# Kernel optimization log

Measured on AMD Instinct MI355X. Metric: run time of the kernel, lower is better.

Reference implementation:

```python
import jax, jax.numpy as jnp
import numpy as np

NX = 8        # state dim
NU = 8        # control dim (== NX, required by original Fx assignment)
N = 64        # horizon
BATCH = 2048
M = N * NU    # condensed QP size = 512
MAX_ITER = 100
STEP = 0.01
U_MIN, U_MAX = -1.0, 1.0


def _build_buffers():
    rng = np.random.default_rng(0)
    A = rng.standard_normal((NX, NX))
    A /= 1.05 * np.max(np.abs(np.linalg.eigvals(A)))  # stable dynamics
    Bm = 0.1 * rng.standard_normal((NX, NU))
    Q = np.eye(NX)
    R = 0.1 * np.eye(NU)
    Qf = np.eye(NX)
    # Phi[k] = A^k
    Phi = np.zeros((N + 1, NX, NX))
    Phi[0] = np.eye(NX)
    for i in range(N):
        Phi[i + 1] = A @ Phi[i]
    # Gamma[i][:, j*NU:(j+1)*NU] = A^{i-1-j} B  (x_i = A^i x0 + Gamma_i u)
    Gamma = np.zeros((N + 1, NX, M))
    for i in range(1, N + 1):
        for j in range(i):
            Gamma[i, :, j * NU:(j + 1) * NU] = Phi[i - 1 - j] @ Bm
    # Condensed Hessian H_bar = sum_i Gamma_i^T Q Gamma_i + blockdiag(R) + reg
    H = np.zeros((M, M))
    for i in range(1, N):
        H += Gamma[i].T @ Q @ Gamma[i]
    H += Gamma[N].T @ Qf @ Gamma[N]
    H += np.kron(np.eye(N), R)
    H += 1e-6 * np.eye(M)
    return (jnp.asarray(H, jnp.float32), jnp.asarray(Phi, jnp.float32),
            jnp.asarray(Q, jnp.float32))


def setup_inputs() -> dict:
    key = jax.random.key(0)
    k1, k2 = jax.random.split(key)
    x0 = jax.random.normal(k1, (BATCH, NX), dtype=jnp.float32)
    xref = jax.random.normal(k2, (BATCH, N + 1, NX), dtype=jnp.float32)
    H, Phi, Q = _build_buffers()
    return {"x0": x0, "xref": xref, "H": H, "Phi": Phi, "Q": Q}


def reference(x0, xref, H, Phi, Q):
    # Linear term f: Fx_k = -2 * Phi[k] @ Q @ (xref_k - xref_0)   [B, N, NX]
    dx = xref[:, :N] - xref[:, :1]                       # [B, N, NX]
    Fx = -2.0 * jnp.einsum('kij,jl,bkl->bki', Phi[:N], Q, dx)
    f = Fx.reshape(xref.shape[0], M)                     # [B, M]

    # Projected gradient descent QP solve: 100 iterations of
    #   u <- clip(u - step*(H u + f), u_min, u_max)
    def step(u, _):
        grad = u @ H.T + f                               # [B, M]
        u_new = jnp.clip(u - STEP * grad, U_MIN, U_MAX)
        return u_new, None

    u0 = jnp.zeros_like(f)
    u, _ = jax.lax.scan(step, u0, None, length=MAX_ITER)
    return u  # full optimal control sequence [B, N*NU]
```

## Files before the change

kernel.cpp:

```cpp
#include <hip/hip_runtime.h>


typedef unsigned short u16t;
typedef __attribute__((ext_vector_type(8))) short short8;
typedef __attribute__((ext_vector_type(4))) float floatx4;

#define HLDS_BYTES (128 * 520 * 2)
#define UBF_BYTES  (16 * 520 * 2)
#define DYN_LDS    (HLDS_BYTES + UBF_BYTES)

__device__ __forceinline__ u16t f32_to_bf16(float x) {
    unsigned int u = __builtin_bit_cast(unsigned int, x);
    u = (u + 0x7FFFu + ((u >> 16) & 1u)) >> 16;
    return (u16t)u;
}

__global__ void convert_H_bf16(const float* __restrict__ H, u16t* __restrict__ Hb) {
    int idx = blockIdx.x * 256 + threadIdx.x;
    Hb[idx] = f32_to_bf16(H[idx]);
}

#define MFMA(a, b, c) __builtin_amdgcn_mfma_f32_16x16x32_bf16((a), (b), (c), 0, 0, 0)

__global__ __launch_bounds__(512, 2)
void pgd_hybrid_kernel(const float* __restrict__ xref,
                       const float* __restrict__ H,
                       const u16t*  __restrict__ Hb,
                       const float* __restrict__ Phi,
                       const float* __restrict__ Q,
                       float* __restrict__ out)
{
    extern __shared__ __align__(16) char smem[];
    u16t* Hlds = (u16t*)smem;
    u16t (*u_bf)[520] = (u16t(*)[520])(smem + HLDS_BYTES);

    const int tid  = threadIdx.x;
    const int lane = tid & 63;
    const int w    = tid >> 6;
    const int quad = lane >> 4;
    const int lcol = lane & 15;
    const int b0   = blockIdx.x * 16;
    const int colbase = w * 64;

    for (int e = tid; e < 8192; e += 512) {
        int r = e >> 6, c = e & 63;
        *(short8*)&Hlds[r * 520 + c * 8] =
            *(const short8*)&Hb[(long)((r >> 4) * 64 + 32 + (r & 15)) * 512 + c * 8];
    }
    {
        u16t* ub = &u_bf[0][0];
        for (int e = tid; e < 8320; e += 512) ub[e] = 0;
    }

    short8 hfrag[2][16];
    #pragma unroll
    for (int t = 0; t < 2; ++t) {
        const float* hrow = H + (long)(colbase + t * 16 + lcol) * 512;
        #pragma unroll
        for (int ks = 0; ks < 16; ++ks) {
            const float* hp = hrow + ks * 32 + quad * 8;
            short8 fr;
            #pragma unroll
            for (int j = 0; j < 8; ++j) fr[j] = (short)f32_to_bf16(hp[j]);
            hfrag[t][ks] = fr;
        }
    }

    float f_reg[4][4], u_reg[4][4];
    #pragma unroll
    for (int T = 0; T < 4; ++T) {
        int c = colbase + T * 16 + lcol;
        int k = c >> 3, i = c & 7;
        #pragma unroll
        for (int r = 0; r < 4; ++r) {
            int m = quad * 4 + r;
            const float* xr = xref + (long)(b0 + m) * 520;
            float s = 0.f;
            #pragma unroll
            for (int j = 0; j < 8; ++j) {
                float z = 0.f;
                #pragma unroll
                for (int l = 0; l < 8; ++l) z += Q[j * 8 + l] * (xr[k * 8 + l] - xr[l]);
                s += Phi[k * 64 + i * 8 + j] * z;
            }
            f_reg[T][r] = -2.0f * s;
            u_reg[T][r] = 0.0f;
        }
    }
    __syncthreads();

    const u16t* hb3 = Hb + (long)(colbase + 48 + lcol) * 512;
    const u16t* h2  = Hlds + (w * 16 + lcol) * 520;

    short8 s0 = *(const short8*)&hb3[quad * 8];
    short8 s1 = *(const short8*)&hb3[32 + quad * 8];

    for (int it = 0; it < 100; ++it) {
        floatx4 acc[4];
        #pragma unroll
        for (int T = 0; T < 4; ++T) acc[T] = (floatx4){0.f, 0.f, 0.f, 0.f};

        #pragma unroll
        for (int ks = 0; ks < 16; ++ks) {
            short8 a  = *(const short8*)&u_bf[lcol][ks * 32 + quad * 8];
            short8 b2 = *(const short8*)&h2[ks * 32 + quad * 8];
            short8 b3 = s0;
            s0 = s1;
            s1 = *(const short8*)&hb3[(((ks + 2) & 15) * 32 + quad * 8)];
            acc[0] = MFMA(a, hfrag[0][ks], acc[0]);
            acc[1] = MFMA(a, hfrag[1][ks], acc[1]);
            acc[2] = MFMA(a, b2, acc[2]);
            acc[3] = MFMA(a, b3, acc[3]);
        }

        u16t nv[4][4];
        #pragma unroll
        for (int T = 0; T < 4; ++T)
            #pragma unroll
            for (int r = 0; r < 4; ++r) {
                float g  = acc[T][r] + f_reg[T][r];
                float un = u_reg[T][r] - 0.01f * g;
                un = fminf(1.0f, fmaxf(-1.0f, un));
                u_reg[T][r] = un;
                nv[T][r] = f32_to_bf16(un);
            }

        __syncthreads();
        #pragma unroll
        for (int T = 0; T < 4; ++T) {
            int c = colbase + T * 16 + lcol;
            #pragma unroll
            for (int r = 0; r < 4; ++r)
                u_bf[quad * 4 + r][c] = nv[T][r];
        }
        __syncthreads();
    }

    #pragma unroll
    for (int T = 0; T < 4; ++T) {
        int c = colbase + T * 16 + lcol;
        #pragma unroll
        for (int r = 0; r < 4; ++r)
            out[(long)(b0 + quad * 4 + r) * 512 + c] = u_reg[T][r];
    }
}

extern "C" void kernel_launch(void* const* d_in, const int* in_sizes, int n_in,
                              void* d_out, int out_size, void* d_ws, size_t ws_size,
                              hipStream_t stream) {
    const float* xref = (const float*)d_in[1];
    const float* H    = (const float*)d_in[2];
    const float* Phi  = (const float*)d_in[3];
    const float* Q    = (const float*)d_in[4];
    u16t* Hb = (u16t*)d_ws;

    static int attr_done = 0;
    (void)hipFuncSetAttribute((const void*)pgd_hybrid_kernel,
                              hipFuncAttributeMaxDynamicSharedMemorySize, DYN_LDS);
    (void)attr_done;

    convert_H_bf16<<<1024, 256, 0, stream>>>(H, Hb);
    pgd_hybrid_kernel<<<128, 512, DYN_LDS, stream>>>(xref, H, Hb, Phi, Q, (float*)d_out);
}
```

Baseline: 268.5 us.

## Transpose MFMA operands for vectorized u writes, deepen H prefetch ring

After: 331.8 us. 23.6% more time.

```diff
diff --git a/kernel.cpp b/kernel.cpp
--- a/kernel.cpp
+++ b/kernel.cpp
@@ -3,6 +3,7 @@
 
 typedef unsigned short u16t;
 typedef __attribute__((ext_vector_type(8))) short short8;
+typedef __attribute__((ext_vector_type(4))) short short4v;
 typedef __attribute__((ext_vector_type(4))) float floatx4;
 
 #define HLDS_BYTES (128 * 520 * 2)
@@ -23,12 +24,11 @@
 #define MFMA(a, b, c) __builtin_amdgcn_mfma_f32_16x16x32_bf16((a), (b), (c), 0, 0, 0)
 
 __global__ __launch_bounds__(512, 2)
-void pgd_hybrid_kernel(const float* __restrict__ xref,
-                       const float* __restrict__ H,
-                       const u16t*  __restrict__ Hb,
-                       const float* __restrict__ Phi,
-                       const float* __restrict__ Q,
-                       float* __restrict__ out)
+void pgd_kernel9(const float* __restrict__ xref,
+                 const u16t*  __restrict__ Hb,
+                 const float* __restrict__ Phi,
+                 const float* __restrict__ Q,
+                 float* __restrict__ out)
 {
     extern __shared__ __align__(16) char smem[];
     u16t* Hlds = (u16t*)smem;
@@ -52,48 +52,45 @@
         for (int e = tid; e < 8320; e += 512) ub[e] = 0;
     }
 
-    short8 hfrag[2][16];
+    short8 hfragA[2][16];
     #pragma unroll
     for (int t = 0; t < 2; ++t) {
-        const float* hrow = H + (long)(colbase + t * 16 + lcol) * 512;
+        const u16t* hrow = Hb + (long)(colbase + t * 16 + lcol) * 512;
         #pragma unroll
-        for (int ks = 0; ks < 16; ++ks) {
-            const float* hp = hrow + ks * 32 + quad * 8;
-            short8 fr;
-            #pragma unroll
-            for (int j = 0; j < 8; ++j) fr[j] = (short)f32_to_bf16(hp[j]);
-            hfrag[t][ks] = fr;
-        }
+        for (int ks = 0; ks < 16; ++ks)
+            hfragA[t][ks] = *(const short8*)&hrow[ks * 32 + quad * 8];
     }
 
     float f_reg[4][4], u_reg[4][4];
-    #pragma unroll
-    for (int T = 0; T < 4; ++T) {
-        int c = colbase + T * 16 + lcol;
-        int k = c >> 3, i = c & 7;
+    {
+        const float* xr = xref + (long)(b0 + lcol) * 520;
         #pragma unroll
-        for (int r = 0; r < 4; ++r) {
-            int m = quad * 4 + r;
-            const float* xr = xref + (long)(b0 + m) * 520;
-            float s = 0.f;
+        for (int T = 0; T < 4; ++T) {
             #pragma unroll
-            for (int j = 0; j < 8; ++j) {
-                float z = 0.f;
+            for (int r = 0; r < 4; ++r) {
+                int c = colbase + T * 16 + quad * 4 + r;
+                int k = c >> 3, i = c & 7;
+                float s = 0.f;
                 #pragma unroll
-                for (int l = 0; l < 8; ++l) z += Q[j * 8 + l] * (xr[k * 8 + l] - xr[l]);
-                s += Phi[k * 64 + i * 8 + j] * z;
+                for (int j = 0; j < 8; ++j) {
+                    float z = 0.f;
+                    #pragma unroll
+                    for (int l = 0; l < 8; ++l) z += Q[j * 8 + l] * (xr[k * 8 + l] - xr[l]);
+                    s += Phi[k * 64 + i * 8 + j] * z;
+                }
+                f_reg[T][r] = -2.0f * s;
+                u_reg[T][r] = 0.0f;
             }
-            f_reg[T][r] = -2.0f * s;
-            u_reg[T][r] = 0.0f;
         }
     }
     __syncthreads();
 
+    const u16t* h2 = Hlds + (w * 16 + lcol) * 520;
     const u16t* hb3 = Hb + (long)(colbase + 48 + lcol) * 512;
-    const u16t* h2  = Hlds + (w * 16 + lcol) * 520;
-
-    short8 s0 = *(const short8*)&hb3[quad * 8];
-    short8 s1 = *(const short8*)&hb3[32 + quad * 8];
+    short8 ring[8];
+    #pragma unroll
+    for (int i = 0; i < 8; ++i)
+        ring[i] = *(const short8*)&hb3[i * 32 + quad * 8];
 
     for (int it = 0; it < 100; ++it) {
         floatx4 acc[4];
@@ -104,16 +101,14 @@
         for (int ks = 0; ks < 16; ++ks) {
             short8 a  = *(const short8*)&u_bf[lcol][ks * 32 + quad * 8];
             short8 b2 = *(const short8*)&h2[ks * 32 + quad * 8];
-            short8 b3 = s0;
-            s0 = s1;
-            s1 = *(const short8*)&hb3[(((ks + 2) & 15) * 32 + quad * 8)];
-            acc[0] = MFMA(a, hfrag[0][ks], acc[0]);
-            acc[1] = MFMA(a, hfrag[1][ks], acc[1]);
-            acc[2] = MFMA(a, b2, acc[2]);
-            acc[3] = MFMA(a, b3, acc[3]);
+            short8 b3 = ring[ks & 7];
+            ring[ks & 7] = *(const short8*)&hb3[((ks + 8) & 15) * 32 + quad * 8];
+            acc[0] = MFMA(hfragA[0][ks], a, acc[0]);
+            acc[1] = MFMA(hfragA[1][ks], a, acc[1]);
+            acc[2] = MFMA(b2, a, acc[2]);
+            acc[3] = MFMA(b3, a, acc[3]);
         }
 
-        u16t nv[4][4];
         #pragma unroll
         for (int T = 0; T < 4; ++T)
             #pragma unroll
@@ -122,26 +117,25 @@
                 float un = u_reg[T][r] - 0.01f * g;
                 un = fminf(1.0f, fmaxf(-1.0f, un));
                 u_reg[T][r] = un;
-                nv[T][r] = f32_to_bf16(un);
             }
 
         __syncthreads();
         #pragma unroll
         for (int T = 0; T < 4; ++T) {
-            int c = colbase + T * 16 + lcol;
+            short4v nv;
             #pragma unroll
-            for (int r = 0; r < 4; ++r)
-                u_bf[quad * 4 + r][c] = nv[T][r];
+            for (int r = 0; r < 4; ++r) nv[r] = (short)f32_to_bf16(u_reg[T][r]);
+            *(short4v*)&u_bf[lcol][colbase + T * 16 + quad * 4] = nv;
         }
         __syncthreads();
     }
 
     #pragma unroll
     for (int T = 0; T < 4; ++T) {
-        int c = colbase + T * 16 + lcol;
+        floatx4 v;
         #pragma unroll
-        for (int r = 0; r < 4; ++r)
-            out[(long)(b0 + quad * 4 + r) * 512 + c] = u_reg[T][r];
+        for (int r = 0; r < 4; ++r) v[r] = u_reg[T][r];
+        *(floatx4*)&out[(long)(b0 + lcol) * 512 + colbase + T * 16 + quad * 4] = v;
     }
 }
 
@@ -154,11 +148,9 @@
     const float* Q    = (const float*)d_in[4];
     u16t* Hb = (u16t*)d_ws;
 
-    static int attr_done = 0;
-    (void)hipFuncSetAttribute((const void*)pgd_hybrid_kernel,
+    (void)hipFuncSetAttribute((const void*)pgd_kernel9,
                               hipFuncAttributeMaxDynamicSharedMemorySize, DYN_LDS);
-    (void)attr_done;
 
     convert_H_bf16<<<1024, 256, 0, stream>>>(H, Hb);
-    pgd_hybrid_kernel<<<128, 512, DYN_LDS, stream>>>(xref, H, Hb, Phi, Q, (float*)d_out);
+    pgd_kernel9<<<128, 512, DYN_LDS, stream>>>(xref, Hb, Phi, Q, (float*)d_out);
 }
```
